# Kernel optimization log

Measured on AMD Instinct MI355X. Metric: run time of the kernel, lower is better.

Reference implementation:

```python
import jax, jax.numpy as jnp
import numpy as np

B, T, F, H, OUT = 128, 512, 1, 512, 1


def setup_inputs() -> dict:
    key = jax.random.key(0)
    ks = jax.random.split(key, 12)
    s1 = 1.0 / np.sqrt(H)  # torch LSTMCell/Linear default init scale
    u = lambda k, shape, s: jax.random.uniform(k, shape, jnp.float32, -s, s)
    return {
        "x": jax.random.normal(ks[0], (B, T), jnp.float32),
        "W_ih1": u(ks[1], (4 * H, F), s1),
        "W_hh1": u(ks[2], (4 * H, H), s1),
        "b_ih1": u(ks[3], (4 * H,), s1),
        "b_hh1": u(ks[4], (4 * H,), s1),
        "W_ih2": u(ks[5], (4 * H, H), s1),
        "W_hh2": u(ks[6], (4 * H, H), s1),
        "b_ih2": u(ks[7], (4 * H,), s1),
        "b_hh2": u(ks[8], (4 * H,), s1),
        "W_out": u(ks[9], (OUT, H), s1),
        "b_out": u(ks[10], (OUT,), s1),
        "future": 32,
    }


def _lstm_cell(x_t, h, c, W_ih, W_hh, b_ih, b_hh):
    # gates: [B, 4H]; torch LSTMCell gate order: i, f, g, o
    gates = x_t @ W_ih.T + b_ih + h @ W_hh.T + b_hh
    i, f, g, o = jnp.split(gates, 4, axis=-1)
    c_new = jax.nn.sigmoid(f) * c + jax.nn.sigmoid(i) * jnp.tanh(g)
    h_new = jax.nn.sigmoid(o) * jnp.tanh(c_new)
    return h_new, c_new


def reference(x, W_ih1, W_hh1, b_ih1, b_hh1, W_ih2, W_hh2, b_ih2, b_hh2,
              W_out, b_out, future):
    bsz = x.shape[0]
    hid = W_hh1.shape[1]
    zeros = jnp.zeros((bsz, hid), x.dtype)

    def run_cells(x_t, h1, c1, h2, c2):
        h1, c1 = _lstm_cell(x_t, h1, c1, W_ih1, W_hh1, b_ih1, b_hh1)
        h2, c2 = _lstm_cell(h1, h2, c2, W_ih2, W_hh2, b_ih2, b_hh2)
        out = h2 @ W_out.T + b_out  # [B, 1]
        return h1, c1, h2, c2, out

    def step(carry, x_t):
        h1, c1, h2, c2 = carry
        h1, c1, h2, c2, out = run_cells(x_t, h1, c1, h2, c2)
        return (h1, c1, h2, c2), out

    xs = jnp.swapaxes(x, 0, 1)[..., None]  # [T, B, 1]
    carry, outs = jax.lax.scan(step, (zeros, zeros, zeros, zeros), xs)

    if future > 0:
        def fstep(carry, _):
            h1, c1, h2, c2, out = carry
            h1, c1, h2, c2, out = run_cells(out, h1, c1, h2, c2)
            return (h1, c1, h2, c2, out), out

        fcarry = (*carry, outs[-1])
        _, fouts = jax.lax.scan(fstep, fcarry, None, length=future)
        outs = jnp.concatenate([outs, fouts], axis=0)  # [T+future, B, 1]

    # stack(dim=1).squeeze(2) -> [B, T+future]
    return jnp.swapaxes(outs, 0, 1)[..., 0]
```

## Files before the change

### kernel.cpp

```cpp
#include <hip/hip_runtime.h>
#include <cstdint>

#define Hdim 512
#define Bdim 128
#define Tdim 512
#define FUT  32
#define TT   (Tdim + FUT)
#define RD   8
#define PD   4
#define FSTR 32
#define CAPIT (1 << 22)

typedef _Float16 f16;
typedef f16      half8  __attribute__((ext_vector_type(8)));
typedef float    f32x4  __attribute__((ext_vector_type(4)));
typedef unsigned long long ull;

#define AW1_OFF  0
#define AW2R_OFF (AW1_OFF + 1048576)
#define AW2I_OFF (AW2R_OFF + 1048576)
#define B1P_OFF  (AW2I_OFF + 1048576)
#define B2P_OFF  (B1P_OFF + 2048)
#define WX1_OFF  (B2P_OFF + 2048)
#define XT_OFF   (WX1_OFF + 2048)
#define H1G_OFF  (XT_OFF + 65536)
#define H2G_OFF  (H1G_OFF + 524288)
#define PB_OFF   (H2G_OFF + 524288)
#define ARR_OFF  (PB_OFF + 1048576)
#define WS_FLOATS (ARR_OFF + 8192)

#define F1Gp(g,i)  (flg + ((g)*32 + (i)) * FSTR)
#define FPp(g,i)   (flg + (64 + (g)*32 + (i)) * FSTR)
#define F2Gp(g,i)  (flg + (128 + (g)*32 + (i)) * FSTR)
#define FOGp(g,q)  (flg + (192 + (g)*4 + (q)) * FSTR)

__device__ __forceinline__ float sigm(float v) { return 1.0f / (1.0f + __expf(-v)); }
__device__ __forceinline__ float tanh_fast(float v) {
    v = fminf(fmaxf(v, -20.0f), 20.0f);
    float e = __expf(2.0f * v);
    return (e - 1.0f) / (e + 1.0f);
}

__device__ __forceinline__ unsigned cohloadu(const unsigned* p) {
    return __hip_atomic_load(p, __ATOMIC_RELAXED, __HIP_MEMORY_SCOPE_AGENT);
}
__device__ __forceinline__ void cohstoreu(unsigned* p, unsigned v) {
    __hip_atomic_store(p, v, __ATOMIC_RELAXED, __HIP_MEMORY_SCOPE_AGENT);
}
__device__ __forceinline__ ull cohload64(const ull* p) {
    return __hip_atomic_load(p, __ATOMIC_RELAXED, __HIP_MEMORY_SCOPE_AGENT);
}
__device__ __forceinline__ void cohstore64(ull* p, ull v) {
    __hip_atomic_store(p, v, __ATOMIC_RELAXED, __HIP_MEMORY_SCOPE_AGENT);
}
union HB  { ull u[2]; half8 h; };
union HB4 { ull u[2]; f32x4 f; };
__device__ __forceinline__ half8 fragload(const half8* p) {
    const ull* q = (const ull*)p;
    HB t; t.u[0] = cohload64(q); t.u[1] = cohload64(q + 1);
    return t.h;
}

__global__ void lstm_prep(const float* __restrict__ x,
                          const float* __restrict__ W_ih1, const float* __restrict__ W_hh1,
                          const float* __restrict__ b_ih1, const float* __restrict__ b_hh1,
                          const float* __restrict__ W_ih2, const float* __restrict__ W_hh2,
                          const float* __restrict__ b_ih2, const float* __restrict__ b_hh2,
                          float* __restrict__ ws, float* __restrict__ out) {
    int i = blockIdx.x * blockDim.x + threadIdx.x;
    f16* aw1  = (f16*)(ws + AW1_OFF);
    f16* aw2r = (f16*)(ws + AW2R_OFF);
    f16* aw2i = (f16*)(ws + AW2I_OFF);

    if (i < 131072) {
        int mt = i >> 10, rest = i & 1023, ks = rest >> 6, lane = rest & 63;
        int m = mt * 16 + (lane & 15);
        int u = m >> 2, g = m & 3;
        int kbase = ks * 32 + (lane >> 4) * 8;
        size_t ohi = ((((size_t)mt * 16 + ks) * 2 + 0) * 64 + lane) * 8;
        size_t olo = ((((size_t)mt * 16 + ks) * 2 + 1) * 64 + lane) * 8;
        #pragma unroll
        for (int j = 0; j < 8; ++j) {
            float wv = W_hh1[(size_t)(g * Hdim + u) * Hdim + kbase + j];
            f16 hi = (f16)wv;
            f16 lo = (f16)(wv - (float)hi);
            aw1[ohi + j] = hi; aw1[olo + j] = lo;
        }
    }
    if (i >= 131072 && i < 262144) {
        int i2 = i - 131072;
        int mt = i2 >> 10, rest = i2 & 1023, ks = rest >> 6, lane = rest & 63;
        int m = mt * 16 + (lane & 15);
        int u = m >> 2, g = m & 3;
        int kbase = ks * 32 + (lane >> 4) * 8;
        size_t ohi = ((((size_t)mt * 16 + ks) * 2 + 0) * 64 + lane) * 8;
        size_t olo = ((((size_t)mt * 16 + ks) * 2 + 1) * 64 + lane) * 8;
        #pragma unroll
        for (int j = 0; j < 8; ++j) {
            float wv = W_hh2[(size_t)(g * Hdim + u) * Hdim + kbase + j];
            f16 hi = (f16)wv;
            f16 lo = (f16)(wv - (float)hi);
            aw2r[ohi + j] = hi; aw2r[olo + j] = lo;
        }
    }
    if (i >= 262144 && i < 393216) {
        int i2 = i - 262144;
        int mt = i2 >> 10, rest = i2 & 1023, ks = rest >> 6, lane = rest & 63;
        int m = mt * 16 + (lane & 15);
        int u = m >> 2, g = m & 3;
        int kbase = ks * 32 + (lane >> 4) * 8;
        size_t ohi = ((((size_t)mt * 16 + ks) * 2 + 0) * 64 + lane) * 8;
        size_t olo = ((((size_t)mt * 16 + ks) * 2 + 1) * 64 + lane) * 8;
        #pragma unroll
        for (int j = 0; j < 8; ++j) {
            float wv = W_ih2[(size_t)(g * Hdim + u) * Hdim + kbase + j];
            f16 hi = (f16)wv;
            f16 lo = (f16)(wv - (float)hi);
            aw2i[ohi + j] = hi; aw2i[olo + j] = lo;
        }
    }
    if (i < Hdim) {
        float4 bb1 = { b_ih1[i] + b_hh1[i],               b_ih1[Hdim+i] + b_hh1[Hdim+i],
                       b_ih1[2*Hdim+i] + b_hh1[2*Hdim+i], b_ih1[3*Hdim+i] + b_hh1[3*Hdim+i] };
        float4 bb2 = { b_ih2[i] + b_hh2[i],               b_ih2[Hdim+i] + b_hh2[Hdim+i],
                       b_ih2[2*Hdim+i] + b_hh2[2*Hdim+i], b_ih2[3*Hdim+i] + b_hh2[3*Hdim+i] };
        float4 wx  = { W_ih1[i], W_ih1[Hdim+i], W_ih1[2*Hdim+i], W_ih1[3*Hdim+i] };
        ((float4*)(ws + B1P_OFF))[i] = bb1;
        ((float4*)(ws + B2P_OFF))[i] = bb2;
        ((float4*)(ws + WX1_OFF))[i] = wx;
    }
    if (i < Tdim * Bdim) {
        int t = i >> 7, b = i & 127;
        ws[XT_OFF + i] = x[b * Tdim + t];
    }
    if (i < 262144) {
        ((ull*)(ws + H1G_OFF))[i] = 0;
        ((ull*)(ws + H2G_OFF))[i] = 0;
        ((ull*)(ws + PB_OFF))[i] = 0;
        ((ull*)(ws + PB_OFF))[262144 + i] = 0;
    }
    if (i < 8192) ((unsigned*)(ws + ARR_OFF))[i] = 0u;
    if (i < Bdim * TT) out[i] = 0.f;
}

__global__ __launch_bounds__(256, 1) void lstm_main(float* ws,
                                                    const float* __restrict__ Wout,
                                                    const float* __restrict__ bout,
                                                    float* __restrict__ out) {
    const int tid  = threadIdx.x;
    const int w    = tid >> 6;
    const int lane = tid & 63;
    const int quad = lane >> 4;
    const int col  = lane & 15;

    __shared__ f16   awlds[65536];
    __shared__ float wout_lds[Hdim];
    __shared__ float psum[4][64];
    __shared__ float xflds[64];
    __shared__ float qpart[4][64];
    __shared__ __align__(16) ull hstg[512];
    __shared__ int sXcd, sOrd, badf;

    unsigned* flg = (unsigned*)(ws + ARR_OFF);
    unsigned short* stg = (unsigned short*)hstg;
    const float* xT = ws + XT_OFF;
    const float bout0 = bout[0];

    if (tid == 0) {
        badf = 0;
        unsigned xcc;
        asm volatile("s_getreg_b32 %0, hwreg(HW_REG_XCC_ID, 0, 32)" : "=s"(xcc));
        xcc &= 0xF;
        sXcd = (int)xcc;
        sOrd = (int)atomicAdd(flg + (200 + xcc) * FSTR, 1u);
    }
    __syncthreads();
    const int xcd = sXcd, ord = sOrd;

    const bool is1   = (xcd < 2);
    const bool is2   = (xcd == 2 || xcd == 3);
    const bool isI   = (xcd == 4 || xcd == 5);
    const bool isout = (xcd == 6) && (ord < 8);
    const bool active = ((is1 || is2 || isI) && ord < 32) || isout;
    if (!active) return;

    const int gA  = is1 ? xcd : is2 ? (xcd - 2) : isI ? (xcd - 4) : (ord >> 2);
    const int oq  = isout ? (ord & 3) : 0;
    const int ntw = gA * 4 + w;
    const int ks1 = ord >> 1, qp0 = (ord & 1) * 2;

    auto h1pf = [&](int par, int spl) {
        return (const half8*)((const unsigned short*)(ws + H1G_OFF) + (size_t)(par*2+spl) * 65536); };
    auto h2pf = [&](int par, int spl) {
        return (const half8*)((const unsigned short*)(ws + H2G_OFF) + (size_t)(par*2+spl) * 65536); };
    auto h1ull = [&](int par, int spl) {
        return (ull*)(ws + H1G_OFF) + (size_t)(par*2+spl) * 16384; };
    auto h2ull = [&](int par, int spl) {
        return (ull*)(ws + H2G_OFF) + (size_t)(par*2+spl) * 16384; };
    auto pidx = [&](int par4, int mt) -> size_t {
        return ((((size_t)par4 * 2 + gA) * 32 + ord) * 16 + (mt * 4 + w)) * 64 + lane;
    };
    ull* Pu = (ull*)(ws + PB_OFF);

    if (is1 || is2 || isI) {
        const half8* s = (const half8*)(ws + (is1 ? AW1_OFF : is2 ? AW2R_OFF : AW2I_OFF))
                       + (size_t)ord * 8192;
        half8* d = (half8*)awlds;
        for (int i = tid; i < 8192; i += 256) d[i] = s[i];
    }
    wout_lds[tid]       = Wout[tid];
    wout_lds[256 + tid] = Wout[256 + tid];
    __syncthreads();

    auto gemm = [&](const half8* fh, const half8* fl, f32x4* acc) {
        half8 rh[16], rl[16];
        #pragma unroll
        for (int ks = 0; ks < 16; ++ks) {
            rh[ks] = fragload(fh + (ntw * 16 + ks) * 64 + lane);
            rl[ks] = fragload(fl + (ntw * 16 + ks) * 64 + lane);
        }
        const half8* aw8 = (const half8*)awlds;
        #pragma unroll
        for (int ks = 0; ks < 16; ++ks) {
            #pragma unroll
            for (int mt = 0; mt < 4; ++mt) {
                half8 ah = aw8[((mt * 16 + ks) * 2 + 0) * 64 + lane];
                half8 al = aw8[((mt * 16 + ks) * 2 + 1) * 64 + lane];
                acc[mt] = __builtin_amdgcn_mfma_f32_16x16x32_f16(ah, rh[ks], acc[mt], 0, 0, 0);
                acc[mt] = __builtin_amdgcn_mfma_f32_16x16x32_f16(al, rh[ks], acc[mt], 0, 0, 0);
                acc[mt] = __builtin_amdgcn_mfma_f32_16x16x32_f16(ah, rl[ks], acc[mt], 0, 0, 0);
            }
        }
    };

    auto stage1 = [&](int mt, float hv) {
        f16 hhi = (f16)hv;
        f16 hlo = (f16)(hv - (float)hhi);
        int mq = mt * 4 + quad, qp = mq >> 3, jj = mq & 7;
        int hi = ((w * 2 + qp) * 16 + col) * 8 + jj;
        stg[hi]        = __builtin_bit_cast(unsigned short, hhi);
        stg[1024 + hi] = __builtin_bit_cast(unsigned short, hlo);
    };
    auto publish = [&](int dpar, bool to1) {
        __syncthreads();
        int f = 2 * tid;
        int spl = f >> 8, rmix = f & 255, ntl = rmix >> 6, rr = rmix & 63;
        int qp = rr >> 5, colp = (rr & 31) >> 1;
        size_t e = (((size_t)(gA * 4 + ntl) * 16 + ks1) * 64 + (qp0 + qp) * 16 + colp) * 2;
        ull* base = (to1 ? h1ull(dpar, spl) : h2ull(dpar, spl)) + e;
        cohstore64(base,     hstg[f]);
        cohstore64(base + 1, hstg[f + 1]);
    };

    if (is1) {
        const int bcol = ntw * 16 + col;
        float4 b1v[4], wxv[4]; float c1s[4];
        #pragma unroll
        for (int mt = 0; mt < 4; ++mt) {
            int u = ord * 16 + mt * 4 + quad;
            b1v[mt] = ((const float4*)(ws + B1P_OFF))[u];
            wxv[mt] = ((const float4*)(ws + WX1_OFF))[u];
            c1s[mt] = 0.f;
        }
        unsigned* myF1 = F1Gp(gA, ord);
        unsigned fPc = (tid < 64 && lane >= 32) ? 0u : 0xFFFFFFFFu;

        auto wait_main = [&](unsigned T1, unsigned TP) {
            if (tid < 64 && !badf) {
                int gd = 0;
                for (;;) {
                    unsigned a = (lane < 32) ? cohloadu(F1Gp(gA, lane)) : 0xFFFFFFFFu;
                    if (lane >= 32 && fPc < TP) fPc = cohloadu(FPp(gA, lane - 32));
                    if (__all(a >= T1 && fPc >= TP)) break;
                    if (++gd > CAPIT) { badf = 1; break; }
                    __builtin_amdgcn_s_sleep(1);
                }
            }
            asm volatile("" ::: "memory");
            __syncthreads();
        };
        auto wait_fut = [&](unsigned T) {
            if (tid < 64 && !badf) {
                int gd = 0;
                for (;;) {
                    unsigned a = (lane < 32) ? cohloadu(F1Gp(gA, lane))
                                             : cohloadu(F2Gp(gA, lane - 32));
                    if (__all(a >= T)) break;
                    if (++gd > CAPIT) { badf = 1; break; }
                    __builtin_amdgcn_s_sleep(2);
                }
            }
            asm volatile("" ::: "memory");
            __syncthreads();
        };
        auto post1 = [&](unsigned v) {
            __syncthreads();
            if (tid == 0) cohstoreu(myF1, v);
        };
        auto l1_step = [&](int spar, int dpar, float xv) {
            f32x4 acc[4] = {};
            gemm(h1pf(spar, 0), h1pf(spar, 1), acc);
            #pragma unroll
            for (int mt = 0; mt < 4; ++mt) {
                f32x4 g = acc[mt];
                float pi = g[0] + b1v[mt].x + wxv[mt].x * xv;
                float pf = g[1] + b1v[mt].y + wxv[mt].y * xv;
                float pg = g[2] + b1v[mt].z + wxv[mt].z * xv;
                float po = g[3] + b1v[mt].w + wxv[mt].w * xv;
                float c = fmaf(sigm(pf), c1s[mt], sigm(pi) * tanh_fast(pg));
                c1s[mt] = c;
                stage1(mt, sigm(po) * tanh_fast(c));
            }
            publish(dpar, true);
        };

        {
            float xv = xT[bcol];
            #pragma unroll
            for (int mt = 0; mt < 4; ++mt) {
                float pi = b1v[mt].x + wxv[mt].x * xv;
                float pg = b1v[mt].z + wxv[mt].z * xv;
                float po = b1v[mt].w + wxv[mt].w * xv;
                float c = sigm(pi) * tanh_fast(pg);
                c1s[mt] = c;
                stage1(mt, sigm(po) * tanh_fast(c));
            }
            publish(0, true);
            post1(1u);
        }
        for (int t = 0; t <= Tdim - 2; ++t) {
            wait_main((unsigned)(t + 1), (t >= 7) ? (unsigned)(t - 6) : 0u);
            l1_step(t & 7, (t + 1) & 7, xT[(t + 1) * Bdim + bcol]);
            post1((unsigned)(t + 2));
        }
        for (int t = Tdim; t < TT; ++t) {
            wait_fut((unsigned)t);
            {
                int bl = tid & 63, kh = tid >> 6;
                int nt2 = gA * 4 + (bl >> 4), nl = bl & 15;
                const half8* ph = h2pf((t - 1) & 7, 0);
                const half8* pl = h2pf((t - 1) & 7, 1);
                float a = 0.f;
                #pragma unroll
                for (int kk = 0; kk < 4; ++kk) {
                    int ks = kh * 4 + kk;
                    #pragma unroll
                    for (int qd = 0; qd < 4; ++qd) {
                        half8 vh = fragload(ph + (nt2 * 16 + ks) * 64 + qd * 16 + nl);
                        half8 vl = fragload(pl + (nt2 * 16 + ks) * 64 + qd * 16 + nl);
                        int ub = ks * 32 + qd * 8;
                        #pragma unroll
                        for (int j = 0; j < 8; ++j)
                            a = fmaf((float)vh[j] + (float)vl[j], wout_lds[ub + j], a);
                    }
                }
                psum[kh][bl] = a;
                __syncthreads();
                if (tid < 64)
                    xflds[tid] = psum[0][tid] + psum[1][tid] + psum[2][tid]
                               + psum[3][tid] + bout0;
                __syncthreads();
            }
            l1_step((t - 1) & 7, t & 7, xflds[bcol & 63]);
            post1((unsigned)(t + 1));
        }
    }
    else if (is2) {
        float c2s[4] = {0.f, 0.f, 0.f, 0.f};
        unsigned* myF2 = F2Gp(gA, ord);
        unsigned* myFP = FPp(gA, ord);
        unsigned fPc2 = (tid < 64 && lane == 0) ? 0u : 0xFFFFFFFFu;
        unsigned fogc = (tid < 64 && lane >= 32 && lane < 36) ? 0u : 0xFFFFFFFFu;

        auto waitP = [&](unsigned T) {
            if (tid < 64 && !badf) {
                int gd = 0;
                for (;;) {
                    if (lane == 0 && fPc2 < T) fPc2 = cohloadu(myFP);
                    if (__all(fPc2 >= T)) break;
                    if (++gd > CAPIT) { badf = 1; break; }
                    __builtin_amdgcn_s_sleep(2);
                }
            }
            asm volatile("" ::: "memory");
            __syncthreads();
        };
        auto waitB = [&](unsigned T2, unsigned To) {
            if (tid < 64 && !badf) {
                int gd = 0;
                for (;;) {
                    unsigned a = (lane < 32) ? cohloadu(F2Gp(gA, lane)) : 0xFFFFFFFFu;
                    if (lane >= 32 && lane < 36 && fogc < To) fogc = cohloadu(FOGp(gA, lane - 32));
                    if (__all(a >= T2 && fogc >= To)) break;
                    if (++gd > CAPIT) { badf = 1; break; }
                    __builtin_amdgcn_s_sleep(1);
                }
            }
            asm volatile("" ::: "memory");
            __syncthreads();
        };

        for (int s = 0; s < TT; ++s) {
            int cpar = s & 7, ppar = (s - 1) & 7;
            waitP((unsigned)(s + 1));
            HB4 praw[4];
            #pragma unroll
            for (int mt = 0; mt < 4; ++mt) {
                const ull* q = Pu + pidx(s & (PD - 1), mt) * 2;
                praw[mt].u[0] = cohload64(q);
                praw[mt].u[1] = cohload64(q + 1);
            }
            waitB((unsigned)s, (s >= 8) ? (unsigned)(s - 7) : 0u);

            f32x4 acc[4] = {};
            if (s > 0) gemm(h2pf(ppar, 0), h2pf(ppar, 1), acc);
            #pragma unroll
            for (int mt = 0; mt < 4; ++mt) {
                f32x4 g = acc[mt];
                f32x4 p = praw[mt].f;
                float pi = g[0] + p[0], pf = g[1] + p[1];
                float pg = g[2] + p[2], po = g[3] + p[3];
                float c = fmaf(sigm(pf), c2s[mt], sigm(pi) * tanh_fast(pg));
                c2s[mt] = c;
                stage1(mt, sigm(po) * tanh_fast(c));
            }
            publish(cpar, false);
            __syncthreads();
            if (tid == 0) cohstoreu(myF2, (unsigned)(s + 1));
        }
    }
    else if (isI) {
        float4 b2v[4];
        #pragma unroll
        for (int mt = 0; mt < 4; ++mt)
            b2v[mt] = ((const float4*)(ws + B2P_OFF))[ord * 16 + mt * 4 + quad];
        unsigned* myFP = FPp(gA, ord);
        unsigned f1c = (tid < 64 && lane < 32) ? 0u : 0xFFFFFFFFu;
        unsigned f2c = (tid < 64 && lane >= 32) ? 0u : 0xFFFFFFFFu;

        auto waitI = [&](unsigned T1, unsigned T2) {
            if (tid < 64 && !badf) {
                int gd = 0;
                for (;;) {
                    if (lane < 32 && f1c < T1) f1c = cohloadu(F1Gp(gA, lane));
                    if (lane >= 32 && f2c < T2) f2c = cohloadu(F2Gp(gA, lane - 32));
                    if (__all(f1c >= T1 && f2c >= T2)) break;
                    if (++gd > CAPIT) { badf = 1; break; }
                    __builtin_amdgcn_s_sleep(2);
                }
            }
            asm volatile("" ::: "memory");
            __syncthreads();
        };

        for (int s = 0; s < TT; ++s) {
            waitI((unsigned)(s + 1), (s >= PD) ? (unsigned)(s - (PD - 1)) : 0u);
            f32x4 acc[4] = {};
            gemm(h1pf(s & 7, 0), h1pf(s & 7, 1), acc);
            #pragma unroll
            for (int mt = 0; mt < 4; ++mt) {
                HB4 p;
                p.f = acc[mt];
                p.f[0] += b2v[mt].x; p.f[1] += b2v[mt].y;
                p.f[2] += b2v[mt].z; p.f[3] += b2v[mt].w;
                ull* q = Pu + pidx(s & (PD - 1), mt) * 2;
                cohstore64(q,     p.u[0]);
                cohstore64(q + 1, p.u[1]);
            }
            __syncthreads();
            if (tid == 0) cohstoreu(myFP, (unsigned)(s + 1));
        }
    }
    else {
        int b = gA * 64 + lane;
        int nt = b >> 4, nl = b & 15;
        int ks = oq * 4 + w;
        unsigned* myFO = FOGp(gA, oq);

        auto waitO = [&](unsigned T) {
            if (tid < 64 && !badf) {
                int gd = 0;
                for (;;) {
                    unsigned a = (lane < 32) ? cohloadu(F2Gp(gA, lane)) : 0xFFFFFFFFu;
                    if (__all(a >= T)) break;
                    if (++gd > CAPIT) { badf = 1; break; }
                    __builtin_amdgcn_s_sleep(2);
                }
            }
            asm volatile("" ::: "memory");
            __syncthreads();
        };

        for (int s = 0; s < TT; ++s) {
            waitO((unsigned)(s + 1));
            const half8* ph = h2pf(s & 7, 0);
            const half8* pl = h2pf(s & 7, 1);
            float a = 0.f;
            #pragma unroll
            for (int qd = 0; qd < 4; ++qd) {
                half8 vh = fragload(ph + (nt * 16 + ks) * 64 + qd * 16 + nl);
                half8 vl = fragload(pl + (nt * 16 + ks) * 64 + qd * 16 + nl);
                int ub = ks * 32 + qd * 8;
                #pragma unroll
                for (int j = 0; j < 8; ++j)
                    a = fmaf((float)vh[j] + (float)vl[j], wout_lds[ub + j], a);
            }
            qpart[w][lane] = a;
            __syncthreads();
            if (w == 0) {
                float v = qpart[0][lane] + qpart[1][lane] + qpart[2][lane] + qpart[3][lane];
                if (oq == 0) v += bout0;
                atomicAdd(&out[(size_t)b * TT + s], v);
            }
            __syncthreads();
            if (tid == 0) cohstoreu(myFO, (unsigned)(s + 1));
        }
    }
}

extern "C" void kernel_launch(void* const* d_in, const int* in_sizes, int n_in,
                              void* d_out, int out_size, void* d_ws, size_t ws_size,
                              hipStream_t stream) {
    const float* x     = (const float*)d_in[0];
    const float* W_ih1 = (const float*)d_in[1];
    const float* W_hh1 = (const float*)d_in[2];
    const float* b_ih1 = (const float*)d_in[3];
    const float* b_hh1 = (const float*)d_in[4];
    const float* W_ih2 = (const float*)d_in[5];
    const float* W_hh2 = (const float*)d_in[6];
    const float* b_ih2 = (const float*)d_in[7];
    const float* b_hh2 = (const float*)d_in[8];
    const float* W_out = (const float*)d_in[9];
    const float* b_out = (const float*)d_in[10];
    float* ws  = (float*)d_ws;
    float* out = (float*)d_out;

    hipLaunchKernelGGL(lstm_prep, dim3(1536), dim3(256), 0, stream,
                       x, W_ih1, W_hh1, b_ih1, b_hh1, W_ih2, W_hh2, b_ih2, b_hh2, ws, out);
    hipLaunchKernelGGL(lstm_main, dim3(256), dim3(256), 0, stream,
                       ws, W_out, b_out, out);
}
```

Baseline: 4.629 ms.

## Fold layer-2 input projection into layer-2 blocks, drop separate I-stage

Removes the dedicated XCD group that computed the layer-2 input GEMM (W_ih2·h1) and passed partial sums through a global P buffer with its own flags. Layer-2 blocks now compute that projection themselves, reading W_ih2 fragments straight from global memory, right after publishing h2 for step s and before waiting on the next recurrence. This removes a cross-block handoff (P-buffer stores and loads plus flag polling) from each timestep. The cost is extra work on the layer-2 critical path, and the W_ih2 reads come from global memory rather than LDS.

Result: slower. 12.72 ms (+174.9%).

```diff
diff --git a/kernel.cpp b/kernel.cpp
--- a/kernel.cpp
+++ b/kernel.cpp
@@ -7,7 +7,6 @@
 #define FUT  32
 #define TT   (Tdim + FUT)
 #define RD   8
-#define PD   4
 #define FSTR 32
 #define CAPIT (1 << 22)
 
@@ -25,12 +24,10 @@
 #define XT_OFF   (WX1_OFF + 2048)
 #define H1G_OFF  (XT_OFF + 65536)
 #define H2G_OFF  (H1G_OFF + 524288)
-#define PB_OFF   (H2G_OFF + 524288)
-#define ARR_OFF  (PB_OFF + 1048576)
+#define ARR_OFF  (H2G_OFF + 524288)
 #define WS_FLOATS (ARR_OFF + 8192)
 
 #define F1Gp(g,i)  (flg + ((g)*32 + (i)) * FSTR)
-#define FPp(g,i)   (flg + (64 + (g)*32 + (i)) * FSTR)
 #define F2Gp(g,i)  (flg + (128 + (g)*32 + (i)) * FSTR)
 #define FOGp(g,q)  (flg + (192 + (g)*4 + (q)) * FSTR)
 
@@ -54,7 +51,6 @@
     __hip_atomic_store(p, v, __ATOMIC_RELAXED, __HIP_MEMORY_SCOPE_AGENT);
 }
 union HB  { ull u[2]; half8 h; };
-union HB4 { ull u[2]; f32x4 f; };
 __device__ __forceinline__ half8 fragload(const half8* p) {
     const ull* q = (const ull*)p;
     HB t; t.u[0] = cohload64(q); t.u[1] = cohload64(q + 1);
@@ -136,8 +132,6 @@
     if (i < 262144) {
         ((ull*)(ws + H1G_OFF))[i] = 0;
         ((ull*)(ws + H2G_OFF))[i] = 0;
-        ((ull*)(ws + PB_OFF))[i] = 0;
-        ((ull*)(ws + PB_OFF))[262144 + i] = 0;
     }
     if (i < 8192) ((unsigned*)(ws + ARR_OFF))[i] = 0u;
     if (i < Bdim * TT) out[i] = 0.f;
@@ -179,12 +173,11 @@
 
     const bool is1   = (xcd < 2);
     const bool is2   = (xcd == 2 || xcd == 3);
-    const bool isI   = (xcd == 4 || xcd == 5);
-    const bool isout = (xcd == 6) && (ord < 8);
-    const bool active = ((is1 || is2 || isI) && ord < 32) || isout;
+    const bool isout = (xcd == 4) && (ord < 8);
+    const bool active = ((is1 || is2) && ord < 32) || isout;
     if (!active) return;
 
-    const int gA  = is1 ? xcd : is2 ? (xcd - 2) : isI ? (xcd - 4) : (ord >> 2);
+    const int gA  = is1 ? xcd : is2 ? (xcd - 2) : (ord >> 2);
     const int oq  = isout ? (ord & 3) : 0;
     const int ntw = gA * 4 + w;
     const int ks1 = ord >> 1, qp0 = (ord & 1) * 2;
@@ -197,14 +190,9 @@
         return (ull*)(ws + H1G_OFF) + (size_t)(par*2+spl) * 16384; };
     auto h2ull = [&](int par, int spl) {
         return (ull*)(ws + H2G_OFF) + (size_t)(par*2+spl) * 16384; };
-    auto pidx = [&](int par4, int mt) -> size_t {
-        return ((((size_t)par4 * 2 + gA) * 32 + ord) * 16 + (mt * 4 + w)) * 64 + lane;
-    };
-    ull* Pu = (ull*)(ws + PB_OFF);
-
-    if (is1 || is2 || isI) {
-        const half8* s = (const half8*)(ws + (is1 ? AW1_OFF : is2 ? AW2R_OFF : AW2I_OFF))
-                       + (size_t)ord * 8192;
+
+    if (is1 || is2) {
+        const half8* s = (const half8*)(ws + (is1 ? AW1_OFF : AW2R_OFF)) + (size_t)ord * 8192;
         half8* d = (half8*)awlds;
         for (int i = tid; i < 8192; i += 256) d[i] = s[i];
     }
@@ -263,15 +251,15 @@
             c1s[mt] = 0.f;
         }
         unsigned* myF1 = F1Gp(gA, ord);
-        unsigned fPc = (tid < 64 && lane >= 32) ? 0u : 0xFFFFFFFFu;
-
-        auto wait_main = [&](unsigned T1, unsigned TP) {
+        unsigned f2c = (tid < 64 && lane >= 32) ? 0u : 0xFFFFFFFFu;
+
+        auto wait_main = [&](unsigned T1, unsigned T2) {
             if (tid < 64 && !badf) {
                 int gd = 0;
                 for (;;) {
                     unsigned a = (lane < 32) ? cohloadu(F1Gp(gA, lane)) : 0xFFFFFFFFu;
-                    if (lane >= 32 && fPc < TP) fPc = cohloadu(FPp(gA, lane - 32));
-                    if (__all(a >= T1 && fPc >= TP)) break;
+                    if (lane >= 32 && f2c < T2) f2c = cohloadu(F2Gp(gA, lane - 32));
+                    if (__all(a >= T1 && f2c >= T2)) break;
                     if (++gd > CAPIT) { badf = 1; break; }
                     __builtin_amdgcn_s_sleep(1);
                 }
@@ -367,19 +355,23 @@
     }
     else if (is2) {
         float c2s[4] = {0.f, 0.f, 0.f, 0.f};
+        float4 b2v[4];
+        #pragma unroll
+        for (int mt = 0; mt < 4; ++mt)
+            b2v[mt] = ((const float4*)(ws + B2P_OFF))[ord * 16 + mt * 4 + quad];
         unsigned* myF2 = F2Gp(gA, ord);
-        unsigned* myFP = FPp(gA, ord);
-        unsigned fPc2 = (tid < 64 && lane == 0) ? 0u : 0xFFFFFFFFu;
+        const half8* wi = (const half8*)(ws + AW2I_OFF) + (size_t)ord * 8192;
+        unsigned f1c  = (tid < 64 && lane < 32) ? 0u : 0xFFFFFFFFu;
         unsigned fogc = (tid < 64 && lane >= 32 && lane < 36) ? 0u : 0xFFFFFFFFu;
 
-        auto waitP = [&](unsigned T) {
+        auto waitF1 = [&](unsigned T) {
             if (tid < 64 && !badf) {
                 int gd = 0;
                 for (;;) {
-                    if (lane == 0 && fPc2 < T) fPc2 = cohloadu(myFP);
-                    if (__all(fPc2 >= T)) break;
+                    if (lane < 32 && f1c < T) f1c = cohloadu(F1Gp(gA, lane));
+                    if (__all(f1c >= T)) break;
                     if (++gd > CAPIT) { badf = 1; break; }
-                    __builtin_amdgcn_s_sleep(2);
+                    __builtin_amdgcn_s_sleep(1);
                 }
             }
             asm volatile("" ::: "memory");
@@ -400,75 +392,59 @@
             __syncthreads();
         };
 
+        f32x4 accP[4];
+        auto gemmP = [&](int spar) {
+            half8 rh[16], rl[16];
+            const half8* fh = h1pf(spar, 0);
+            const half8* fl = h1pf(spar, 1);
+            #pragma unroll
+            for (int ks = 0; ks < 16; ++ks) {
+                rh[ks] = fragload(fh + (ntw * 16 + ks) * 64 + lane);
+                rl[ks] = fragload(fl + (ntw * 16 + ks) * 64 + lane);
+            }
+            #pragma unroll
+            for (int ks = 0; ks < 16; ++ks) {
+                #pragma unroll
+                for (int mt = 0; mt < 4; ++mt) {
+                    half8 ah = wi[((mt * 16 + ks) * 2 + 0) * 64 + lane];
+                    half8 al = wi[((mt * 16 + ks) * 2 + 1) * 64 + lane];
+                    accP[mt] = __builtin_amdgcn_mfma_f32_16x16x32_f16(ah, rh[ks], accP[mt], 0, 0, 0);
+                    accP[mt] = __builtin_amdgcn_mfma_f32_16x16x32_f16(al, rh[ks], accP[mt], 0, 0, 0);
+                    accP[mt] = __builtin_amdgcn_mfma_f32_16x16x32_f16(ah, rl[ks], accP[mt], 0, 0, 0);
+                }
+            }
+        };
+
+        waitF1(1u);
+        #pragma unroll
+        for (int mt = 0; mt < 4; ++mt)
+            accP[mt] = (f32x4){b2v[mt].x, b2v[mt].y, b2v[mt].z, b2v[mt].w};
+        gemmP(0);
+
         for (int s = 0; s < TT; ++s) {
-            int cpar = s & 7, ppar = (s - 1) & 7;
-            waitP((unsigned)(s + 1));
-            HB4 praw[4];
-            #pragma unroll
-            for (int mt = 0; mt < 4; ++mt) {
-                const ull* q = Pu + pidx(s & (PD - 1), mt) * 2;
-                praw[mt].u[0] = cohload64(q);
-                praw[mt].u[1] = cohload64(q + 1);
-            }
             waitB((unsigned)s, (s >= 8) ? (unsigned)(s - 7) : 0u);
-
             f32x4 acc[4] = {};
-            if (s > 0) gemm(h2pf(ppar, 0), h2pf(ppar, 1), acc);
+            if (s > 0) gemm(h2pf((s - 1) & 7, 0), h2pf((s - 1) & 7, 1), acc);
             #pragma unroll
             for (int mt = 0; mt < 4; ++mt) {
                 f32x4 g = acc[mt];
-                f32x4 p = praw[mt].f;
+                f32x4 p = accP[mt];
                 float pi = g[0] + p[0], pf = g[1] + p[1];
                 float pg = g[2] + p[2], po = g[3] + p[3];
                 float c = fmaf(sigm(pf), c2s[mt], sigm(pi) * tanh_fast(pg));
                 c2s[mt] = c;
                 stage1(mt, sigm(po) * tanh_fast(c));
             }
-            publish(cpar, false);
+            publish(s & 7, false);
             __syncthreads();
             if (tid == 0) cohstoreu(myF2, (unsigned)(s + 1));
-        }
-    }
-    else if (isI) {
-        float4 b2v[4];
-        #pragma unroll
-        for (int mt = 0; mt < 4; ++mt)
-            b2v[mt] = ((const float4*)(ws + B2P_OFF))[ord * 16 + mt * 4 + quad];
-        unsigned* myFP = FPp(gA, ord);
-        unsigned f1c = (tid < 64 && lane < 32) ? 0u : 0xFFFFFFFFu;
-        unsigned f2c = (tid < 64 && lane >= 32) ? 0u : 0xFFFFFFFFu;
-
-        auto waitI = [&](unsigned T1, unsigned T2) {
-            if (tid < 64 && !badf) {
-                int gd = 0;
-                for (;;) {
-                    if (lane < 32 && f1c < T1) f1c = cohloadu(F1Gp(gA, lane));
-                    if (lane >= 32 && f2c < T2) f2c = cohloadu(F2Gp(gA, lane - 32));
-                    if (__all(f1c >= T1 && f2c >= T2)) break;
-                    if (++gd > CAPIT) { badf = 1; break; }
-                    __builtin_amdgcn_s_sleep(2);
-                }
-            }
-            asm volatile("" ::: "memory");
-            __syncthreads();
-        };
-
-        for (int s = 0; s < TT; ++s) {
-            waitI((unsigned)(s + 1), (s >= PD) ? (unsigned)(s - (PD - 1)) : 0u);
-            f32x4 acc[4] = {};
-            gemm(h1pf(s & 7, 0), h1pf(s & 7, 1), acc);
-            #pragma unroll
-            for (int mt = 0; mt < 4; ++mt) {
-                HB4 p;
-                p.f = acc[mt];
-                p.f[0] += b2v[mt].x; p.f[1] += b2v[mt].y;
-                p.f[2] += b2v[mt].z; p.f[3] += b2v[mt].w;
-                ull* q = Pu + pidx(s & (PD - 1), mt) * 2;
-                cohstore64(q,     p.u[0]);
-                cohstore64(q + 1, p.u[1]);
-            }
-            __syncthreads();
-            if (tid == 0) cohstoreu(myFP, (unsigned)(s + 1));
+            if (s + 1 < TT) {
+                waitF1((unsigned)(s + 2));
+                #pragma unroll
+                for (int mt = 0; mt < 4; ++mt)
+                    accP[mt] = (f32x4){b2v[mt].x, b2v[mt].y, b2v[mt].z, b2v[mt].w};
+                gemmP((s + 1) & 7);
+            }
         }
     }
     else {
```
